# Kernel tuning notes

Hardware: AMD Instinct MI355X
Metric: run time of the kernel (lower is better)

## Reference

```python
import jax, jax.numpy as jnp
import numpy as np

N = 50000      # nodes
E = 500000     # edges
CHAN = 64      # channels
R0 = 2.0       # radial cutoff scale


def radial_encode_8(d, r0):
    # d: (E,) edge distances -> (E, 8) Gaussian radial basis on [0, r0]
    mu = jnp.linspace(0.0, r0, 8).astype(d.dtype)
    sigma = r0 / 8.0
    return jnp.exp(-(((d[:, None] - mu) / sigma) ** 2))


def vector_sigmoid(v):
    # v: (..., 3, chan); sigmoid-shaped vector activation (norm over spatial axis)
    vv = jnp.sum(v * v, axis=-2, keepdims=True)
    return v / jnp.sqrt(1.0 + vv)


def setup_inputs() -> dict:
    key = jax.random.key(0)
    ks = jax.random.split(key, 12)
    rn = lambda i, shape, scale=1.0: jax.random.normal(ks[i], shape, jnp.float32) * scale
    src = jax.random.randint(ks[0], (E,), 0, N)
    dst = jax.random.randint(ks[1], (E,), 0, N)
    r_ij = rn(2, (E, 3))
    z_0 = rn(3, (N, CHAN))
    z_1 = rn(4, (N, 3, CHAN))
    emb = rn(5, (N, CHAN))
    k = CHAN ** -0.5
    return dict(
        src=src, dst=dst, r_ij=r_ij, z_0=z_0, z_1=z_1, emb=emb,
        W_enc=rn(6, (8, CHAN), 8 ** -0.5), b_enc=jnp.zeros((CHAN,), jnp.float32),
        W_src=rn(7, (CHAN, CHAN), k), b_src=jnp.zeros((CHAN,), jnp.float32),
        W_dst=rn(8, (CHAN, CHAN), k), b_dst=jnp.zeros((CHAN,), jnp.float32),
        W_gate=rn(9, (CHAN, 4 * CHAN), k), b_gate=jnp.zeros((4 * CHAN,), jnp.float32),
        W_s=rn(10, (CHAN, CHAN), k), W_v=rn(11, (CHAN, CHAN), k),
    )


def reference(src, dst, r_ij, z_0, z_1, emb,
              W_enc, b_enc, W_src, b_src, W_dst, b_dst,
              W_gate, b_gate, W_s, W_v):
    # edges_read: gather node embeddings to edges, fuse src/dst linears
    emb_ij = (emb[src] @ W_src + b_src) + (emb[dst] @ W_dst + b_dst)        # (E, C)
    d = jnp.sqrt(jnp.sum(r_ij * r_ij, axis=-1))                              # (E,)
    dist_emb = radial_encode_8(d, R0) @ W_enc + b_enc + emb_ij               # (E, C)
    # vector sigmoid on scaled displacement
    r_hat = vector_sigmoid((r_ij * (7.0 / R0))[..., None])[..., 0]           # (E, 3)
    # edges_read_dst: gather dst-node scalar/vector features
    z0_j = z_0[dst]                                                          # (E, C)
    z1_j = z_1[dst]                                                          # (E, 3, C)
    # MessageContract (rank-1 equivariant tensor contraction, gated by dist_emb)
    g = (dist_emb @ W_gate + b_gate).reshape(E, 4, CHAN)                     # (E, 4, C)
    s_msg = g[:, 0] * z0_j + g[:, 1] * jnp.einsum('ei,eic->ec', r_hat, z1_j)  # scalar msg
    psi0 = s_msg @ W_s                                                        # (E, C)
    v_msg = g[:, 2][:, None, :] * z1_j \
          + g[:, 3][:, None, :] * (r_hat[:, :, None] * z0_j[:, None, :])     # (E, 3, C)
    psi1 = jnp.einsum('eic,cd->eid', v_msg, W_v)                              # (E, 3, C)
    # edges_reduce_src: scatter-add messages back to source nodes
    out0 = jax.ops.segment_sum(psi0, src, num_segments=N)                     # (N, C)
    out1 = jax.ops.segment_sum(psi1.reshape(E, 3 * CHAN), src,
                               num_segments=N).reshape(N, 3, CHAN)            # (N, 3, C)
    return out0, out1
```

## Files before the change

kernel.cpp:

```cpp
#include <hip/hip_runtime.h>

typedef unsigned int u32;
typedef _Float16 h16;
typedef __attribute__((ext_vector_type(4))) _Float16 h4;

#define WS_WSG   0
#define WS_WEG   32768
#define WS_BALL  34816
#define WS_GS    35328

__global__ void zero_k(float* p, int n) {
    int i = blockIdx.x * blockDim.x + threadIdx.x;
    int st = gridDim.x * blockDim.x;
    for (; i < n; i += st) p[i] = 0.0f;
}

__global__ void compose_k(const float* __restrict__ Wsrc, const float* __restrict__ Wdst,
                          const float* __restrict__ Wenc, const float* __restrict__ benc,
                          const float* __restrict__ bsrc, const float* __restrict__ bdst,
                          const float* __restrict__ Wgate, const float* __restrict__ bgate,
                          float* __restrict__ ws) {
    const int j = threadIdx.x;
    const int r = blockIdx.x;
    const int p = ((j & 63) << 2) + (j >> 6);
    if (r < 64) {
        float a = 0.f, b = 0.f;
        for (int c = 0; c < 64; ++c) {
            const float wg = Wgate[c * 256 + j];
            a += Wsrc[r * 64 + c] * wg;
            b += Wdst[r * 64 + c] * wg;
        }
        ws[WS_WSG + r * 512 + p] = a;
        ws[WS_WSG + r * 512 + 256 + p] = b;
    } else if (r < 72) {
        const int m = r - 64;
        float a = 0.f;
        for (int c = 0; c < 64; ++c) a += Wenc[m * 64 + c] * Wgate[c * 256 + j];
        ws[WS_WEG + m * 256 + j] = a;
    } else {
        float a = bgate[j];
        for (int c = 0; c < 64; ++c)
            a += (benc[c] + bsrc[c] + bdst[c]) * Wgate[c * 256 + j];
        ws[WS_BALL + j] = a;
    }
}

__global__ __launch_bounds__(512, 1) void nodepre3_k(
    const float* __restrict__ emb, const float* __restrict__ Wc,
    h16* __restrict__ HG, int N) {
    __shared__ __align__(16) float sW[32768];
    __shared__ __align__(16) float sEm[1024];
    for (int i = threadIdx.x * 4; i < 32768; i += 2048)
        *(float4*)&sW[i] = *(const float4*)&Wc[i];

    const int c4 = (threadIdx.x & 127) << 2;
    const int g = threadIdx.x >> 7;
    const int lim = N * 64;
    const int ntiles = (N + 15) >> 4;

    for (int tile = blockIdx.x; tile < ntiles; tile += gridDim.x) {
        const int n0 = tile << 4;
        const int base = n0 * 64;
        __syncthreads();
        for (int i = threadIdx.x * 4; i < 1024; i += 2048) {
            const int gi = base + i;
            *(float4*)&sEm[i] = (gi < lim) ? *(const float4*)&emb[gi]
                                           : make_float4(0.f, 0.f, 0.f, 0.f);
        }
        __syncthreads();

        float4 a0 = {0,0,0,0}, a1 = {0,0,0,0}, a2 = {0,0,0,0}, a3 = {0,0,0,0};
        const float* e0p = &sEm[(g * 4 + 0) * 64];
        const float* e1p = &sEm[(g * 4 + 1) * 64];
        const float* e2p = &sEm[(g * 4 + 2) * 64];
        const float* e3p = &sEm[(g * 4 + 3) * 64];
        #pragma unroll 8
        for (int k = 0; k < 64; ++k) {
            const float4 w = *(const float4*)&sW[k * 512 + c4];
            const float e0 = e0p[k], e1 = e1p[k], e2 = e2p[k], e3 = e3p[k];
            a0.x += e0 * w.x; a0.y += e0 * w.y; a0.z += e0 * w.z; a0.w += e0 * w.w;
            a1.x += e1 * w.x; a1.y += e1 * w.y; a1.z += e1 * w.z; a1.w += e1 * w.w;
            a2.x += e2 * w.x; a2.y += e2 * w.y; a2.z += e2 * w.z; a2.w += e2 * w.w;
            a3.x += e3 * w.x; a3.y += e3 * w.y; a3.z += e3 * w.z; a3.w += e3 * w.w;
        }
        const int nb = n0 + g * 4;
        const h4 h0 = { (h16)a0.x, (h16)a0.y, (h16)a0.z, (h16)a0.w };
        const h4 h1 = { (h16)a1.x, (h16)a1.y, (h16)a1.z, (h16)a1.w };
        const h4 h2 = { (h16)a2.x, (h16)a2.y, (h16)a2.z, (h16)a2.w };
        const h4 h3 = { (h16)a3.x, (h16)a3.y, (h16)a3.z, (h16)a3.w };
        if (nb + 0 < N) *(h4*)&HG[(size_t)(nb + 0) * 512 + c4] = h0;
        if (nb + 1 < N) *(h4*)&HG[(size_t)(nb + 1) * 512 + c4] = h1;
        if (nb + 2 < N) *(h4*)&HG[(size_t)(nb + 2) * 512 + c4] = h2;
        if (nb + 3 < N) *(h4*)&HG[(size_t)(nb + 3) * 512 + c4] = h3;
    }
}

__global__ void hz_k(const float* __restrict__ z0g, const float* __restrict__ z1g,
                     h16* __restrict__ HZ, int N) {
    const int tot = N * 64;
    for (int idx = blockIdx.x * blockDim.x + threadIdx.x; idx < tot;
         idx += gridDim.x * blockDim.x) {
        const int n = idx >> 6, l = idx & 63;
        const h4 v = { (h16)z1g[n * 192 + l], (h16)z1g[n * 192 + 64 + l],
                       (h16)z1g[n * 192 + 128 + l], (h16)z0g[n * 64 + l] };
        *(h4*)&HZ[(size_t)n * 256 + (l << 2)] = v;
    }
}

__global__ __launch_bounds__(256, 8) void edge_h16_k(
    const int* __restrict__ src, const int* __restrict__ dst,
    const float* __restrict__ r_ij, const h16* __restrict__ HG,
    const h16* __restrict__ HZ, const float* __restrict__ WeG,
    const float* __restrict__ ball, float* __restrict__ out, int N, int E) {
    __shared__ float sWe[2048];
    __shared__ float sBall[256];
    __shared__ int sFl[2];

    if (threadIdx.x == 0) {
        const u32* ps = (const u32*)src;
        const u32* pd = (const u32*)dst;
        int s64 = 1, d64 = 1;
        for (int i = 1; i < 128; i += 2) {
            if (ps[i] != 0u) s64 = 0;
            if (pd[i] != 0u) d64 = 0;
        }
        sFl[0] = s64;
        sFl[1] = d64;
    }
    for (int i = threadIdx.x; i < 2048; i += 256) sWe[i] = WeG[i];
    sBall[threadIdx.x] = ball[threadIdx.x];
    __syncthreads();

    const int wid = threadIdx.x >> 6, lane = threadIdx.x & 63;
    const int i64s = sFl[0], i64d = sFl[1];

    const float bl0 = sBall[lane], bl1 = sBall[64 + lane];
    const float bl2 = sBall[128 + lane], bl3 = sBall[192 + lane];

    for (int e = blockIdx.x * 4 + wid; e < E; e += gridDim.x * 4) {
        const int s = i64s ? src[2 * e] : src[e];
        const int t = i64d ? dst[2 * e] : dst[e];
        if (s < 0 || s >= N || t < 0 || t >= N) continue;

        const h4 gsv = *(const h4*)&HG[(size_t)s * 512 + (lane << 2)];
        const h4 gdv = *(const h4*)&HG[(size_t)t * 512 + 256 + (lane << 2)];
        const h4 zv  = *(const h4*)&HZ[(size_t)t * 256 + (lane << 2)];
        const float r0 = r_ij[e * 3 + 0];
        const float r1 = r_ij[e * 3 + 1];
        const float r2 = r_ij[e * 3 + 2];

        float g0 = (float)gsv.x + (float)gdv.x + bl0;
        float g1 = (float)gsv.y + (float)gdv.y + bl1;
        float g2 = (float)gsv.z + (float)gdv.z + bl2;
        float g3 = (float)gsv.w + (float)gdv.w + bl3;
        const float za = (float)zv.x, zb = (float)zv.y, zc = (float)zv.z;
        const float z0v = (float)zv.w;

        const float d = sqrtf(r0 * r0 + r1 * r1 + r2 * r2);
        #pragma unroll
        for (int m = 0; m < 8; ++m) {
            const float mu = 0.28571428571f * (float)m;
            const float tt = (d - mu) * 4.0f;
            const float rm = __expf(-tt * tt);
            const float* wq = &sWe[(m << 8) + lane];
            g0 += rm * wq[0];
            g1 += rm * wq[64];
            g2 += rm * wq[128];
            g3 += rm * wq[192];
        }

        const float v0 = r0 * 3.5f, v1 = r1 * 3.5f, v2 = r2 * 3.5f;
        const float inv = rsqrtf(1.0f + v0 * v0 + v1 * v1 + v2 * v2);
        const float h0 = v0 * inv, h1 = v1 * inv, h2 = v2 * inv;
        const float uu = h0 * za + h1 * zb + h2 * zc;

        const float smsg = g0 * z0v + g1 * uu;
        const float vm0 = g2 * za + g3 * h0 * z0v;
        const float vm1 = g2 * zb + g3 * h1 * z0v;
        const float vm2 = g2 * zc + g3 * h2 * z0v;

        atomicAdd(&out[s * 64 + lane], smsg);
        const int bo = N * 64 + s * 192 + lane;
        atomicAdd(&out[bo], vm0);
        atomicAdd(&out[bo + 64], vm1);
        atomicAdd(&out[bo + 128], vm2);
    }
}

__global__ __launch_bounds__(256, 3) void nodepost3_k(
    float* __restrict__ out, const float* __restrict__ Ws,
    const float* __restrict__ Wv, int N) {
    __shared__ __align__(16) float sW[8192];
    __shared__ float sR[64 * 65];
    for (int i = threadIdx.x * 4; i < 8192; i += 1024) {
        *(float4*)&sW[i] = (i < 4096) ? *(const float4*)&Ws[i]
                                      : *(const float4*)&Wv[i - 4096];
    }
    const int c4 = (threadIdx.x & 15) << 2;
    const int rq = threadIdx.x >> 4;
    const int totalRows = 4 * N;
    const int lim = totalRows * 64;
    const int ntiles = (totalRows + 63) >> 6;

    for (int tile = blockIdx.x; tile < ntiles; tile += gridDim.x) {
        const int r0 = tile << 6;
        __syncthreads();
        for (int i = threadIdx.x; i < 4096; i += 256) {
            const int gi = r0 * 64 + i;
            sR[(i >> 6) * 65 + (i & 63)] = (gi < lim) ? out[gi] : 0.f;
        }
        __syncthreads();

        const int rb = rq << 2;
        const int gr = r0 + rb;
        const int o0 = (gr + 0 < N) ? 0 : 4096;
        const int o3 = (gr + 3 < N) ? 0 : 4096;
        float4 a0 = {0,0,0,0}, a1 = {0,0,0,0}, a2 = {0,0,0,0}, a3 = {0,0,0,0};
        const float* rp0 = &sR[(rb + 0) * 65];
        const float* rp1 = &sR[(rb + 1) * 65];
        const float* rp2 = &sR[(rb + 2) * 65];
        const float* rp3 = &sR[(rb + 3) * 65];
        if (o0 == o3) {
            const float* wb = &sW[o0 + c4];
            #pragma unroll 8
            for (int k = 0; k < 64; ++k) {
                const float4 w = *(const float4*)&wb[k * 64];
                const float e0 = rp0[k], e1 = rp1[k], e2 = rp2[k], e3 = rp3[k];
                a0.x += e0 * w.x; a0.y += e0 * w.y; a0.z += e0 * w.z; a0.w += e0 * w.w;
                a1.x += e1 * w.x; a1.y += e1 * w.y; a1.z += e1 * w.z; a1.w += e1 * w.w;
                a2.x += e2 * w.x; a2.y += e2 * w.y; a2.z += e2 * w.z; a2.w += e2 * w.w;
                a3.x += e3 * w.x; a3.y += e3 * w.y; a3.z += e3 * w.z; a3.w += e3 * w.w;
            }
        } else {
            const int o1 = (gr + 1 < N) ? 0 : 4096;
            const int o2 = (gr + 2 < N) ? 0 : 4096;
            #pragma unroll 4
            for (int k = 0; k < 64; ++k) {
                const float4 w0 = *(const float4*)&sW[o0 + k * 64 + c4];
                const float4 w1 = *(const float4*)&sW[o1 + k * 64 + c4];
                const float4 w2 = *(const float4*)&sW[o2 + k * 64 + c4];
                const float4 w3 = *(const float4*)&sW[o3 + k * 64 + c4];
                const float e0 = rp0[k], e1 = rp1[k], e2 = rp2[k], e3 = rp3[k];
                a0.x += e0 * w0.x; a0.y += e0 * w0.y; a0.z += e0 * w0.z; a0.w += e0 * w0.w;
                a1.x += e1 * w1.x; a1.y += e1 * w1.y; a1.z += e1 * w1.z; a1.w += e1 * w1.w;
                a2.x += e2 * w2.x; a2.y += e2 * w2.y; a2.z += e2 * w2.z; a2.w += e2 * w2.w;
                a3.x += e3 * w3.x; a3.y += e3 * w3.y; a3.z += e3 * w3.z; a3.w += e3 * w3.w;
            }
        }
        if (gr + 0 < totalRows) *(float4*)&out[(size_t)(gr + 0) * 64 + c4] = a0;
        if (gr + 1 < totalRows) *(float4*)&out[(size_t)(gr + 1) * 64 + c4] = a1;
        if (gr + 2 < totalRows) *(float4*)&out[(size_t)(gr + 2) * 64 + c4] = a2;
        if (gr + 3 < totalRows) *(float4*)&out[(size_t)(gr + 3) * 64 + c4] = a3;
    }
}

__global__ __launch_bounds__(512, 1) void edge_k(
    const int* __restrict__ src, const int* __restrict__ dst,
    const float* __restrict__ r_ij, const float* __restrict__ z0g,
    const float* __restrict__ z1g, const float* __restrict__ emb,
    const float* __restrict__ Wenc, const float* __restrict__ benc,
    const float* __restrict__ Wsrc, const float* __restrict__ bsrc,
    const float* __restrict__ Wdst, const float* __restrict__ bdst,
    const float* __restrict__ Wgate, const float* __restrict__ bgate,
    const float* __restrict__ Ws, const float* __restrict__ Wv,
    float* __restrict__ out, int N, int E)
{
    __shared__ float sWsrc[4096];
    __shared__ float sWdst[4096];
    __shared__ float sWg[16384];
    __shared__ float sWs[4096];
    __shared__ float sWv[4096];
    __shared__ float sWe[512];
    __shared__ float sB[64];
    __shared__ float sBg[256];
    __shared__ int sFl[2];

    if (threadIdx.x == 0) {
        const u32* ps = (const u32*)src;
        const u32* pd = (const u32*)dst;
        int s64 = 1, d64 = 1;
        for (int i = 1; i < 128; i += 2) {
            if (ps[i] != 0u) s64 = 0;
            if (pd[i] != 0u) d64 = 0;
        }
        sFl[0] = s64;
        sFl[1] = d64;
    }
    for (int i = threadIdx.x; i < 4096; i += 512) {
        sWsrc[i] = Wsrc[i];
        sWdst[i] = Wdst[i];
        sWs[i] = Ws[i];
        sWv[i] = Wv[i];
    }
    for (int i = threadIdx.x; i < 16384; i += 512) sWg[i] = Wgate[i];
    for (int i = threadIdx.x; i < 512; i += 512) sWe[i] = Wenc[i];
    if (threadIdx.x < 64)
        sB[threadIdx.x] = benc[threadIdx.x] + bsrc[threadIdx.x] + bdst[threadIdx.x];
    if (threadIdx.x < 256) sBg[threadIdx.x] = bgate[threadIdx.x];
    __syncthreads();

    const int wid = threadIdx.x >> 6, lane = threadIdx.x & 63;
    const int i64s = sFl[0], i64d = sFl[1];

    for (int e = blockIdx.x * 8 + wid; e < E; e += gridDim.x * 8) {
        const int s = i64s ? src[2 * e] : src[e];
        const int t = i64d ? dst[2 * e] : dst[e];
        if (s < 0 || s >= N || t < 0 || t >= N) continue;

        const float es = emb[s * 64 + lane];
        const float et = emb[t * 64 + lane];
        float de = sB[lane];
        #pragma unroll 8
        for (int k = 0; k < 64; ++k) {
            de += __shfl(es, k, 64) * sWsrc[(k << 6) + lane];
            de += __shfl(et, k, 64) * sWdst[(k << 6) + lane];
        }
        const float r0 = r_ij[e * 3 + 0];
        const float r1 = r_ij[e * 3 + 1];
        const float r2 = r_ij[e * 3 + 2];
        const float d = sqrtf(r0 * r0 + r1 * r1 + r2 * r2);
        #pragma unroll
        for (int m = 0; m < 8; ++m) {
            const float mu = (2.0f / 7.0f) * (float)m;
            const float tt = (d - mu) * 4.0f;
            de += __expf(-tt * tt) * sWe[m * 64 + lane];
        }

        const float v0 = r0 * 3.5f, v1 = r1 * 3.5f, v2 = r2 * 3.5f;
        const float inv = rsqrtf(1.0f + v0 * v0 + v1 * v1 + v2 * v2);
        const float h0 = v0 * inv, h1 = v1 * inv, h2 = v2 * inv;

        const float z0v = z0g[t * 64 + lane];
        const float za = z1g[t * 192 + lane];
        const float zb = z1g[t * 192 + 64 + lane];
        const float zc = z1g[t * 192 + 128 + lane];
        const float uu = h0 * za + h1 * zb + h2 * zc;

        float g0 = sBg[lane], g1 = sBg[64 + lane], g2 = sBg[128 + lane], g3 = sBg[192 + lane];
        #pragma unroll 8
        for (int k = 0; k < 64; ++k) {
            const float dk = __shfl(de, k, 64);
            const float* w = &sWg[(k << 8) + lane];
            g0 += dk * w[0];
            g1 += dk * w[64];
            g2 += dk * w[128];
            g3 += dk * w[192];
        }

        const float smsg = g0 * z0v + g1 * uu;
        const float vm0 = g2 * za + g3 * h0 * z0v;
        const float vm1 = g2 * zb + g3 * h1 * z0v;
        const float vm2 = g2 * zc + g3 * h2 * z0v;

        float p0 = 0.f, q0 = 0.f, q1 = 0.f, q2 = 0.f;
        #pragma unroll 8
        for (int k = 0; k < 64; ++k) {
            const float sk = __shfl(smsg, k, 64);
            const float a = __shfl(vm0, k, 64);
            const float b = __shfl(vm1, k, 64);
            const float c = __shfl(vm2, k, 64);
            p0 += sk * sWs[(k << 6) + lane];
            const float wv = sWv[(k << 6) + lane];
            q0 += a * wv;
            q1 += b * wv;
            q2 += c * wv;
        }

        atomicAdd(&out[s * 64 + lane], p0);
        const int b1 = N * 64 + s * 192 + lane;
        atomicAdd(&out[b1], q0);
        atomicAdd(&out[b1 + 64], q1);
        atomicAdd(&out[b1 + 128], q2);
    }
}

extern "C" void kernel_launch(void* const* d_in, const int* in_sizes, int n_in,
                              void* d_out, int out_size, void* d_ws, size_t ws_size,
                              hipStream_t stream) {
    const int* src = (const int*)d_in[0];
    const int* dst = (const int*)d_in[1];
    const float* r_ij = (const float*)d_in[2];
    const float* z0g  = (const float*)d_in[3];
    const float* z1g  = (const float*)d_in[4];
    const float* emb  = (const float*)d_in[5];
    const float* Wenc = (const float*)d_in[6];
    const float* benc = (const float*)d_in[7];
    const float* Wsrc = (const float*)d_in[8];
    const float* bsrc = (const float*)d_in[9];
    const float* Wdst = (const float*)d_in[10];
    const float* bdst = (const float*)d_in[11];
    const float* Wgate = (const float*)d_in[12];
    const float* bgate = (const float*)d_in[13];
    const float* Ws = (const float*)d_in[14];
    const float* Wv = (const float*)d_in[15];

    const int N = out_size / 256;
    int E = in_sizes[0];
    if (in_sizes[2] / 3 < E) E = in_sizes[2] / 3;

    zero_k<<<2048, 256, 0, stream>>>((float*)d_out, out_size);

    float* ws = (float*)d_ws;
    const size_t need = ((size_t)WS_GS + (size_t)N * 384u + 16u) * sizeof(float);

    if (ws != nullptr && ws_size >= need) {
        compose_k<<<73, 256, 0, stream>>>(Wsrc, Wdst, Wenc, benc, bsrc, bdst,
                                          Wgate, bgate, ws);
        h16* HG = (h16*)(ws + WS_GS);
        h16* HZ = HG + (size_t)N * 512;
        nodepre3_k<<<256, 512, 0, stream>>>(emb, ws + WS_WSG, HG, N);
        hz_k<<<1024, 256, 0, stream>>>(z0g, z1g, HZ, N);
        edge_h16_k<<<2048, 256, 0, stream>>>(src, dst, r_ij, HG, HZ,
                                             ws + WS_WEG, ws + WS_BALL,
                                             (float*)d_out, N, E);
        nodepost3_k<<<2048, 256, 0, stream>>>((float*)d_out, Ws, Wv, N);
    } else {
        edge_k<<<2048, 512, 0, stream>>>(src, dst, r_ij, z0g, z1g, emb, Wenc, benc,
                                         Wsrc, bsrc, Wdst, bdst, Wgate, bgate, Ws, Wv,
                                         (float*)d_out, N, E);
    }
}
```

Baseline: 676.2 us.

## Accumulate edge messages with packed fp16 atomics into interleaved scratch buffer

Replaces the four fp32 atomicAdds per lane per edge with two packed fp16 atomic adds (global_atomic_pk_add_f16) into a node-interleaved half-precision accumulator in workspace. The node post-projection kernel is rewritten to read this interleaved fp16 layout, de-interleave it into shared memory, and write the scalar and vector outputs to their fp32 locations. Zeroing now targets the smaller accumulator instead of the full output. This halves atomic traffic and count, but fp16 accumulation across many edges per node loses precision and risks overflow or tolerance failures.

```diff
diff --git a/kernel.cpp b/kernel.cpp
--- a/kernel.cpp
+++ b/kernel.cpp
@@ -2,12 +2,20 @@
 
 typedef unsigned int u32;
 typedef _Float16 h16;
+typedef __attribute__((ext_vector_type(2))) _Float16 h2;
 typedef __attribute__((ext_vector_type(4))) _Float16 h4;
 
 #define WS_WSG   0
 #define WS_WEG   32768
 #define WS_BALL  34816
 #define WS_GS    35328
+
+__device__ __forceinline__ void pk_add(h16* addr, float lo, float hi) {
+    union { h2 h; u32 u; } cv;
+    cv.h = (h2){ (h16)lo, (h16)hi };
+    asm volatile("global_atomic_pk_add_f16 %0, %1, off sc1"
+                 :: "v"(addr), "v"(cv.u) : "memory");
+}
 
 __global__ void zero_k(float* p, int n) {
     int i = blockIdx.x * blockDim.x + threadIdx.x;
@@ -86,11 +94,11 @@
         const int nb = n0 + g * 4;
         const h4 h0 = { (h16)a0.x, (h16)a0.y, (h16)a0.z, (h16)a0.w };
         const h4 h1 = { (h16)a1.x, (h16)a1.y, (h16)a1.z, (h16)a1.w };
-        const h4 h2 = { (h16)a2.x, (h16)a2.y, (h16)a2.z, (h16)a2.w };
+        const h4 h2v = { (h16)a2.x, (h16)a2.y, (h16)a2.z, (h16)a2.w };
         const h4 h3 = { (h16)a3.x, (h16)a3.y, (h16)a3.z, (h16)a3.w };
         if (nb + 0 < N) *(h4*)&HG[(size_t)(nb + 0) * 512 + c4] = h0;
         if (nb + 1 < N) *(h4*)&HG[(size_t)(nb + 1) * 512 + c4] = h1;
-        if (nb + 2 < N) *(h4*)&HG[(size_t)(nb + 2) * 512 + c4] = h2;
+        if (nb + 2 < N) *(h4*)&HG[(size_t)(nb + 2) * 512 + c4] = h2v;
         if (nb + 3 < N) *(h4*)&HG[(size_t)(nb + 3) * 512 + c4] = h3;
     }
 }
@@ -107,11 +115,11 @@
     }
 }
 
-__global__ __launch_bounds__(256, 8) void edge_h16_k(
+__global__ __launch_bounds__(256, 8) void edge_pk_k(
     const int* __restrict__ src, const int* __restrict__ dst,
     const float* __restrict__ r_ij, const h16* __restrict__ HG,
     const h16* __restrict__ HZ, const float* __restrict__ WeG,
-    const float* __restrict__ ball, float* __restrict__ out, int N, int E) {
+    const float* __restrict__ ball, h16* __restrict__ ACC, int N, int E) {
     __shared__ float sWe[2048];
     __shared__ float sBall[256];
     __shared__ int sFl[2];
@@ -179,17 +187,15 @@
         const float vm1 = g2 * zb + g3 * h1 * z0v;
         const float vm2 = g2 * zc + g3 * h2 * z0v;
 
-        atomicAdd(&out[s * 64 + lane], smsg);
-        const int bo = N * 64 + s * 192 + lane;
-        atomicAdd(&out[bo], vm0);
-        atomicAdd(&out[bo + 64], vm1);
-        atomicAdd(&out[bo + 128], vm2);
-    }
-}
-
-__global__ __launch_bounds__(256, 3) void nodepost3_k(
-    float* __restrict__ out, const float* __restrict__ Ws,
-    const float* __restrict__ Wv, int N) {
+        h16* ap = &ACC[(size_t)s * 256 + (lane << 2)];
+        pk_add(ap,     smsg, vm0);
+        pk_add(ap + 2, vm1,  vm2);
+    }
+}
+
+__global__ __launch_bounds__(256, 3) void nodepost4_k(
+    const h16* __restrict__ ACC, float* __restrict__ out,
+    const float* __restrict__ Ws, const float* __restrict__ Wv, int N) {
     __shared__ __align__(16) float sW[8192];
     __shared__ float sR[64 * 65];
     for (int i = threadIdx.x * 4; i < 8192; i += 1024) {
@@ -198,59 +204,52 @@
     }
     const int c4 = (threadIdx.x & 15) << 2;
     const int rq = threadIdx.x >> 4;
-    const int totalRows = 4 * N;
-    const int lim = totalRows * 64;
-    const int ntiles = (totalRows + 63) >> 6;
+    const int lim = N * 256;
+    const int ntiles = (N + 15) >> 4;
 
     for (int tile = blockIdx.x; tile < ntiles; tile += gridDim.x) {
-        const int r0 = tile << 6;
+        const int n0 = tile << 4;
+        const int base = n0 * 256;
         __syncthreads();
-        for (int i = threadIdx.x; i < 4096; i += 256) {
-            const int gi = r0 * 64 + i;
-            sR[(i >> 6) * 65 + (i & 63)] = (gi < lim) ? out[gi] : 0.f;
+        for (int i = threadIdx.x * 4; i < 4096; i += 1024) {
+            const int nl = i >> 8;
+            const int k = (i & 255) >> 2;
+            h4 v = { (h16)0.f, (h16)0.f, (h16)0.f, (h16)0.f };
+            if (base + i < lim) v = *(const h4*)&ACC[base + i];
+            sR[(nl) * 65 + k] = (float)v.x;
+            sR[(16 + nl) * 65 + k] = (float)v.y;
+            sR[(32 + nl) * 65 + k] = (float)v.z;
+            sR[(48 + nl) * 65 + k] = (float)v.w;
         }
         __syncthreads();
 
         const int rb = rq << 2;
-        const int gr = r0 + rb;
-        const int o0 = (gr + 0 < N) ? 0 : 4096;
-        const int o3 = (gr + 3 < N) ? 0 : 4096;
+        const int part = rb >> 4;
+        const float* wb = &sW[(part == 0 ? 0 : 4096) + c4];
         float4 a0 = {0,0,0,0}, a1 = {0,0,0,0}, a2 = {0,0,0,0}, a3 = {0,0,0,0};
         const float* rp0 = &sR[(rb + 0) * 65];
         const float* rp1 = &sR[(rb + 1) * 65];
         const float* rp2 = &sR[(rb + 2) * 65];
         const float* rp3 = &sR[(rb + 3) * 65];
-        if (o0 == o3) {
-            const float* wb = &sW[o0 + c4];
-            #pragma unroll 8
-            for (int k = 0; k < 64; ++k) {
-                const float4 w = *(const float4*)&wb[k * 64];
-                const float e0 = rp0[k], e1 = rp1[k], e2 = rp2[k], e3 = rp3[k];
-                a0.x += e0 * w.x; a0.y += e0 * w.y; a0.z += e0 * w.z; a0.w += e0 * w.w;
-                a1.x += e1 * w.x; a1.y += e1 * w.y; a1.z += e1 * w.z; a1.w += e1 * w.w;
-                a2.x += e2 * w.x; a2.y += e2 * w.y; a2.z += e2 * w.z; a2.w += e2 * w.w;
-                a3.x += e3 * w.x; a3.y += e3 * w.y; a3.z += e3 * w.z; a3.w += e3 * w.w;
-            }
-        } else {
-            const int o1 = (gr + 1 < N) ? 0 : 4096;
-            const int o2 = (gr + 2 < N) ? 0 : 4096;
-            #pragma unroll 4
-            for (int k = 0; k < 64; ++k) {
-                const float4 w0 = *(const float4*)&sW[o0 + k * 64 + c4];
-                const float4 w1 = *(const float4*)&sW[o1 + k * 64 + c4];
-                const float4 w2 = *(const float4*)&sW[o2 + k * 64 + c4];
-                const float4 w3 = *(const float4*)&sW[o3 + k * 64 + c4];
-                const float e0 = rp0[k], e1 = rp1[k], e2 = rp2[k], e3 = rp3[k];
-                a0.x += e0 * w0.x; a0.y += e0 * w0.y; a0.z += e0 * w0.z; a0.w += e0 * w0.w;
-                a1.x += e1 * w1.x; a1.y += e1 * w1.y; a1.z += e1 * w1.z; a1.w += e1 * w1.w;
-                a2.x += e2 * w2.x; a2.y += e2 * w2.y; a2.z += e2 * w2.z; a2.w += e2 * w2.w;
-                a3.x += e3 * w3.x; a3.y += e3 * w3.y; a3.z += e3 * w3.z; a3.w += e3 * w3.w;
-            }
-        }
-        if (gr + 0 < totalRows) *(float4*)&out[(size_t)(gr + 0) * 64 + c4] = a0;
-        if (gr + 1 < totalRows) *(float4*)&out[(size_t)(gr + 1) * 64 + c4] = a1;
-        if (gr + 2 < totalRows) *(float4*)&out[(size_t)(gr + 2) * 64 + c4] = a2;
-        if (gr + 3 < totalRows) *(float4*)&out[(size_t)(gr + 3) * 64 + c4] = a3;
+        #pragma unroll 8
+        for (int k = 0; k < 64; ++k) {
+            const float4 w = *(const float4*)&wb[k * 64];
+            const float e0 = rp0[k], e1 = rp1[k], e2 = rp2[k], e3 = rp3[k];
+            a0.x += e0 * w.x; a0.y += e0 * w.y; a0.z += e0 * w.z; a0.w += e0 * w.w;
+            a1.x += e1 * w.x; a1.y += e1 * w.y; a1.z += e1 * w.z; a1.w += e1 * w.w;
+            a2.x += e2 * w.x; a2.y += e2 * w.y; a2.z += e2 * w.z; a2.w += e2 * w.w;
+            a3.x += e3 * w.x; a3.y += e3 * w.y; a3.z += e3 * w.z; a3.w += e3 * w.w;
+        }
+        #pragma unroll
+        for (int i = 0; i < 4; ++i) {
+            const int n = n0 + ((rb + i) & 15);
+            if (n >= N) continue;
+            const float4 av = (i == 0) ? a0 : (i == 1) ? a1 : (i == 2) ? a2 : a3;
+            if (part == 0)
+                *(float4*)&out[(size_t)n * 64 + c4] = av;
+            else
+                *(float4*)&out[(size_t)N * 64 + (size_t)n * 192 + (part - 1) * 64 + c4] = av;
+        }
     }
 }
 
@@ -398,23 +397,24 @@
     int E = in_sizes[0];
     if (in_sizes[2] / 3 < E) E = in_sizes[2] / 3;
 
-    zero_k<<<2048, 256, 0, stream>>>((float*)d_out, out_size);
-
     float* ws = (float*)d_ws;
-    const size_t need = ((size_t)WS_GS + (size_t)N * 384u + 16u) * sizeof(float);
+    const size_t need = ((size_t)WS_GS + (size_t)N * 512u + 16u) * sizeof(float);
 
     if (ws != nullptr && ws_size >= need) {
         compose_k<<<73, 256, 0, stream>>>(Wsrc, Wdst, Wenc, benc, bsrc, bdst,
                                           Wgate, bgate, ws);
         h16* HG = (h16*)(ws + WS_GS);
         h16* HZ = HG + (size_t)N * 512;
+        h16* ACC = HZ + (size_t)N * 256;
+        zero_k<<<1024, 256, 0, stream>>>((float*)ACC, N * 128);
         nodepre3_k<<<256, 512, 0, stream>>>(emb, ws + WS_WSG, HG, N);
         hz_k<<<1024, 256, 0, stream>>>(z0g, z1g, HZ, N);
-        edge_h16_k<<<2048, 256, 0, stream>>>(src, dst, r_ij, HG, HZ,
-                                             ws + WS_WEG, ws + WS_BALL,
-                                             (float*)d_out, N, E);
-        nodepost3_k<<<2048, 256, 0, stream>>>((float*)d_out, Ws, Wv, N);
+        edge_pk_k<<<2048, 256, 0, stream>>>(src, dst, r_ij, HG, HZ,
+                                            ws + WS_WEG, ws + WS_BALL,
+                                            ACC, N, E);
+        nodepost4_k<<<2048, 256, 0, stream>>>(ACC, (float*)d_out, Ws, Wv, N);
     } else {
+        zero_k<<<2048, 256, 0, stream>>>((float*)d_out, out_size);
         edge_k<<<2048, 512, 0, stream>>>(src, dst, r_ij, z0g, z1g, emb, Wenc, benc,
                                          Wsrc, bsrc, Wdst, bdst, Wgate, bgate, Ws, Wv,
                                          (float*)d_out, N, E);
```

After: 673.1 us. About the same (-0.5%).
